# Kernel optimization log

Measured on AMD Instinct MI355X. Metric: run time of the kernel, lower is better.

Reference implementation:

```python
import jax, jax.numpy as jnp
import numpy as np

B, N, F, T = 16, 2048, 64, 32  # batch, nodes, features, frames


def setup_inputs() -> dict:
    key = jax.random.key(0)
    ks = jax.random.split(key, 6)
    return {
        "x": jax.random.normal(ks[0], (B, N, F, T), dtype=jnp.float32),
        "U_1": jax.random.normal(ks[1], (N,), dtype=jnp.float32),
        "U_2": jax.random.normal(ks[2], (F, N), dtype=jnp.float32),
        "U_3": jax.random.normal(ks[3], (F,), dtype=jnp.float32),
        "b_e": jax.random.normal(ks[4], (1, T, T), dtype=jnp.float32),
        "V_e": jax.random.normal(ks[5], (T, T), dtype=jnp.float32),
    }


def reference(x, U_1, U_2, U_3, b_e, V_e):
    # lhs = x.permute(0,3,2,1) @ U_1 @ U_2 : (B,T,F,N)@(N,)->(B,T,F); @(F,N)->(B,T,N)
    lhs = jnp.einsum("bnft,n->btf", x, U_1)
    lhs = jnp.einsum("btf,fm->btm", lhs, U_2)
    # rhs = U_3 @ x.permute(2,0,1,3) : (F,)@(F,B,N,T) -> (B,N,T)
    rhs = jnp.einsum("f,bnft->bnt", U_3, x)
    # product : (B,T,N) @ (B,N,T) -> (B,T,T)
    product = jnp.einsum("btn,bns->bts", lhs, rhs)
    # the two chained permutes in the source compose to identity
    E = jnp.einsum("ut,bts->bus", V_e, jax.nn.sigmoid(product + b_e))  # (B,T,T)
    # stable softmax-like normalization over dim=1 (the original's intent)
    E = E - jnp.max(E, axis=1, keepdims=True)
    expE = jnp.exp(E)
    return expE / jnp.sum(expE, axis=1, keepdims=True)
```

## Files before the change

kernel.cpp:

```cpp
#include <hip/hip_runtime.h>
#include <math.h>


#define BDIM 16
#define NDIM 2048
#define FDIM 64
#define TDIM 32
#define GPB  32
#define NC   16

__global__ __launch_bounds__(256) void k1_pass(
    const float* __restrict__ x, const float* __restrict__ U1,
    const float* __restrict__ U3, float* __restrict__ rhs_ws,
    float* __restrict__ lhs_part) {
  const int b    = blockIdx.x / GPB;
  const int gb   = blockIdx.x % GPB;
  const int tid  = threadIdx.x;
  const int wave = tid >> 6;
  const int lane = tid & 63;
  const int frow = lane >> 3;
  const int t4   = (lane & 7) * 4;

  float u3v[8];
#pragma unroll
  for (int i = 0; i < 8; ++i) u3v[i] = U3[frow + 8 * i];

  float4 lacc[8];
#pragma unroll
  for (int i = 0; i < 8; ++i) lacc[i] = make_float4(0.f, 0.f, 0.f, 0.f);

  const int wb = gb * 4 + wave;
  for (int n = wb; n < NDIM; n += GPB * 4) {
    const float* base = x + ((size_t)(b * NDIM + n)) * (FDIM * TDIM);
    const float u1n = U1[n];
    float4 racc = make_float4(0.f, 0.f, 0.f, 0.f);
#pragma unroll
    for (int i = 0; i < 8; ++i) {
      const float4 v = *(const float4*)(base + (frow + 8 * i) * TDIM + t4);
      lacc[i].x = fmaf(u1n, v.x, lacc[i].x);
      lacc[i].y = fmaf(u1n, v.y, lacc[i].y);
      lacc[i].z = fmaf(u1n, v.z, lacc[i].z);
      lacc[i].w = fmaf(u1n, v.w, lacc[i].w);
      racc.x = fmaf(u3v[i], v.x, racc.x);
      racc.y = fmaf(u3v[i], v.y, racc.y);
      racc.z = fmaf(u3v[i], v.z, racc.z);
      racc.w = fmaf(u3v[i], v.w, racc.w);
    }
#pragma unroll
    for (int m = 8; m <= 32; m <<= 1) {
      racc.x += __shfl_xor(racc.x, m, 64);
      racc.y += __shfl_xor(racc.y, m, 64);
      racc.z += __shfl_xor(racc.z, m, 64);
      racc.w += __shfl_xor(racc.w, m, 64);
    }
    if (frow == 0) {
      *(float4*)(rhs_ws + ((size_t)(b * NDIM + n)) * TDIM + t4) = racc;
    }
  }

  __shared__ __align__(16) float sred[4 * 2048];
  float* my = sred + wave * 2048;
#pragma unroll
  for (int i = 0; i < 8; ++i)
    *(float4*)(my + (frow + 8 * i) * TDIM + t4) = lacc[i];
  __syncthreads();
  float* outp = lhs_part + ((size_t)(b * GPB + gb)) * 2048;
  for (int p = tid; p < 2048; p += 256)
    outp[p] = sred[p] + sred[2048 + p] + sred[4096 + p] + sred[6144 + p];
}

__global__ __launch_bounds__(256) void k2_r2(
    const float* __restrict__ rhs_ws, const float* __restrict__ U2,
    const float* __restrict__ lhs_part, float* __restrict__ R2_part,
    float* __restrict__ lhs1) {
  const int b  = blockIdx.x >> 4;
  const int nc = blockIdx.x & 15;
  const int tid = threadIdx.x;

  __shared__ float srhsT[32 * 130];
  __shared__ float sU2[64 * 129];
  __shared__ __align__(16) float sAcc[4 * 2048];

  const float* rbase = rhs_ws + ((size_t)b * NDIM + nc * 128) * TDIM;
  for (int i = tid; i < 1024; i += 256) {
    const float4 v = ((const float4*)rbase)[i];
    const int n  = i >> 3;
    const int s0 = (i & 7) * 4;
    srhsT[(s0 + 0) * 130 + n] = v.x;
    srhsT[(s0 + 1) * 130 + n] = v.y;
    srhsT[(s0 + 2) * 130 + n] = v.z;
    srhsT[(s0 + 3) * 130 + n] = v.w;
  }
  const float* ubase = U2 + nc * 128;
  for (int i = tid; i < 2048; i += 256) {
    const int f = i >> 5, c = (i & 31) * 4;
    const float4 u = *(const float4*)(ubase + (size_t)f * NDIM + c);
    sU2[f * 129 + c + 0] = u.x;
    sU2[f * 129 + c + 1] = u.y;
    sU2[f * 129 + c + 2] = u.z;
    sU2[f * 129 + c + 3] = u.w;
  }

  if (tid < 128) {
    const float* lpb = lhs_part + (size_t)b * GPB * 2048 + nc * 128 + tid;
    float s = 0.f;
#pragma unroll
    for (int g = 0; g < GPB; ++g) s += lpb[g * 2048];
    lhs1[b * 2048 + nc * 128 + tid] = s;
  }
  __syncthreads();

  const int lane = tid & 63;
  const int nsub = tid >> 6;
  const int f0 = (lane >> 2) * 4;
  const int s0 = (lane & 3) * 8;
  float acc[4][8];
#pragma unroll
  for (int k = 0; k < 4; ++k)
#pragma unroll
    for (int m = 0; m < 8; ++m) acc[k][m] = 0.f;

  for (int nn = 0; nn < 32; ++nn) {
    const int n = nsub * 32 + nn;
    float u[4], v[8];
#pragma unroll
    for (int k = 0; k < 4; ++k) u[k] = sU2[(f0 + k) * 129 + n];
#pragma unroll
    for (int m = 0; m < 8; ++m) v[m] = srhsT[(s0 + m) * 130 + n];
#pragma unroll
    for (int k = 0; k < 4; ++k)
#pragma unroll
      for (int m = 0; m < 8; ++m) acc[k][m] = fmaf(u[k], v[m], acc[k][m]);
  }
#pragma unroll
  for (int k = 0; k < 4; ++k)
#pragma unroll
    for (int m = 0; m < 8; ++m)
      sAcc[nsub * 2048 + (f0 + k) * 32 + s0 + m] = acc[k][m];
  __syncthreads();

  float4* dst = (float4*)(R2_part + ((size_t)(b * NC + nc)) * 2048);
  const float4* sa = (const float4*)sAcc;
  for (int i = tid; i < 512; i += 256) {
    float4 r0 = sa[i], r1 = sa[512 + i], r2 = sa[1024 + i], r3 = sa[1536 + i];
    r0.x += r1.x + r2.x + r3.x;
    r0.y += r1.y + r2.y + r3.y;
    r0.z += r1.z + r2.z + r3.z;
    r0.w += r1.w + r2.w + r3.w;
    dst[i] = r0;
  }
}

__global__ __launch_bounds__(1024) void k3(
    const float* __restrict__ lhs1, const float* __restrict__ R2_part,
    const float* __restrict__ b_e, const float* __restrict__ V_e,
    float* __restrict__ out) {
  const int b = blockIdx.x;
  const int tid = threadIdx.x;
  __shared__ float sl[2048], sR[2048];
  __shared__ float sS[1024], sE[1024], sVe[1024], sbe[1024];
  __shared__ float smax[32], ssum[32];

  for (int p = tid; p < 2048; p += 1024) sl[p] = lhs1[b * 2048 + p];
  if (tid < 512) {
    const float* rpb = R2_part + (size_t)b * NC * 2048;
    float4 a = make_float4(0.f, 0.f, 0.f, 0.f);
#pragma unroll
    for (int nc = 0; nc < NC; ++nc) {
      const float4 v = *(const float4*)(rpb + nc * 2048 + tid * 4);
      a.x += v.x; a.y += v.y; a.z += v.z; a.w += v.w;
    }
    *(float4*)(sR + tid * 4) = a;
  }
  sVe[tid] = V_e[tid];
  sbe[tid] = b_e[tid];
  __syncthreads();

  const int t = tid >> 5, s = tid & 31;
  float p = 0.f;
#pragma unroll
  for (int f = 0; f < FDIM; ++f) p = fmaf(sl[f * 32 + t], sR[f * 32 + s], p);
  sS[t * 32 + s] = 1.f / (1.f + expf(-(p + sbe[t * 32 + s])));
  __syncthreads();
  float e = 0.f;
#pragma unroll
  for (int tt = 0; tt < 32; ++tt) e = fmaf(sVe[t * 32 + tt], sS[tt * 32 + s], e);
  sE[t * 32 + s] = e;
  __syncthreads();
  if (tid < 32) {
    float m = -1e30f;
    for (int uu = 0; uu < 32; ++uu) m = fmaxf(m, sE[uu * 32 + tid]);
    float sum = 0.f;
    for (int uu = 0; uu < 32; ++uu) sum += expf(sE[uu * 32 + tid] - m);
    smax[tid] = m;
    ssum[tid] = sum;
  }
  __syncthreads();
  out[b * 1024 + t * 32 + s] = expf(sE[t * 32 + s] - smax[s]) / ssum[s];
}

extern "C" void kernel_launch(void* const* d_in, const int* in_sizes, int n_in,
                              void* d_out, int out_size, void* d_ws, size_t ws_size,
                              hipStream_t stream) {
  const float* x   = (const float*)d_in[0];
  const float* U1  = (const float*)d_in[1];
  const float* U2  = (const float*)d_in[2];
  const float* U3  = (const float*)d_in[3];
  const float* b_e = (const float*)d_in[4];
  const float* V_e = (const float*)d_in[5];
  float* out = (float*)d_out;
  float* ws  = (float*)d_ws;

  float* rhs_ws   = ws;
  float* lhs_part = ws + 1048576;
  float* R2_part  = ws + 2097152;
  float* lhs1     = ws + 2097152 + 524288;

  k1_pass<<<BDIM * GPB, 256, 0, stream>>>(x, U1, U3, rhs_ws, lhs_part);
  k2_r2<<<BDIM * NC, 256, 0, stream>>>(rhs_ws, U2, lhs_part, R2_part, lhs1);
  k3<<<BDIM, 1024, 0, stream>>>(lhs1, R2_part, b_e, V_e, out);
}
```

Before: 386.4 us.

## Fuse final sigmoid/softmax stage into k2 via last-block atomic counter

Removes the third kernel launch by having the last block to finish each batch in k2 (detected with a per-batch atomic counter reset in k1) reduce the R2 partials and compute the sigmoid, V_e mix and column softmax. The goal is to save one launch and its gap. The tail work now runs on 256 threads instead of 1024, and the threadfence/atomic adds a little synchronisation cost.

```diff
diff --git a/kernel.cpp b/kernel.cpp
--- a/kernel.cpp
+++ b/kernel.cpp
@@ -12,7 +12,9 @@
 __global__ __launch_bounds__(256) void k1_pass(
     const float* __restrict__ x, const float* __restrict__ U1,
     const float* __restrict__ U3, float* __restrict__ rhs_ws,
-    float* __restrict__ lhs_part) {
+    float* __restrict__ lhs_part, int* __restrict__ batch_cnt) {
+  if (blockIdx.x == 0 && threadIdx.x < BDIM) batch_cnt[threadIdx.x] = 0;
+
   const int b    = blockIdx.x / GPB;
   const int gb   = blockIdx.x % GPB;
   const int tid  = threadIdx.x;
@@ -69,10 +71,12 @@
     outp[p] = sred[p] + sred[2048 + p] + sred[4096 + p] + sred[6144 + p];
 }
 
-__global__ __launch_bounds__(256) void k2_r2(
+__global__ __launch_bounds__(256) void k2_fused(
     const float* __restrict__ rhs_ws, const float* __restrict__ U2,
     const float* __restrict__ lhs_part, float* __restrict__ R2_part,
-    float* __restrict__ lhs1) {
+    float* __restrict__ lhs1, int* __restrict__ batch_cnt,
+    const float* __restrict__ b_e, const float* __restrict__ V_e,
+    float* __restrict__ out) {
   const int b  = blockIdx.x >> 4;
   const int nc = blockIdx.x & 15;
   const int tid = threadIdx.x;
@@ -80,6 +84,10 @@
   __shared__ float srhsT[32 * 130];
   __shared__ float sU2[64 * 129];
   __shared__ __align__(16) float sAcc[4 * 2048];
+  __shared__ __align__(16) float sl[2048], sR[2048];
+  __shared__ float sS[1024], sE[1024], sVe[1024], sbe[1024];
+  __shared__ float smax[32], ssum[32];
+  __shared__ int isLast;
 
   const float* rbase = rhs_ws + ((size_t)b * NDIM + nc * 128) * TDIM;
   for (int i = tid; i < 1024; i += 256) {
@@ -149,43 +157,51 @@
     r0.w += r1.w + r2.w + r3.w;
     dst[i] = r0;
   }
-}
-
-__global__ __launch_bounds__(1024) void k3(
-    const float* __restrict__ lhs1, const float* __restrict__ R2_part,
-    const float* __restrict__ b_e, const float* __restrict__ V_e,
-    float* __restrict__ out) {
-  const int b = blockIdx.x;
-  const int tid = threadIdx.x;
-  __shared__ float sl[2048], sR[2048];
-  __shared__ float sS[1024], sE[1024], sVe[1024], sbe[1024];
-  __shared__ float smax[32], ssum[32];
-
-  for (int p = tid; p < 2048; p += 1024) sl[p] = lhs1[b * 2048 + p];
-  if (tid < 512) {
-    const float* rpb = R2_part + (size_t)b * NC * 2048;
+
+  __threadfence();
+  __syncthreads();
+  if (tid == 0) {
+    const int old = atomicAdd(&batch_cnt[b], 1);
+    isLast = (old == NC - 1) ? 1 : 0;
+  }
+  __syncthreads();
+  if (!isLast) return;
+  __threadfence();
+
+  const float* rpb = R2_part + (size_t)b * NC * 2048;
+  for (int i = tid; i < 512; i += 256) {
     float4 a = make_float4(0.f, 0.f, 0.f, 0.f);
 #pragma unroll
-    for (int nc = 0; nc < NC; ++nc) {
-      const float4 v = *(const float4*)(rpb + nc * 2048 + tid * 4);
+    for (int c = 0; c < NC; ++c) {
+      const float4 v = *(const float4*)(rpb + c * 2048 + i * 4);
       a.x += v.x; a.y += v.y; a.z += v.z; a.w += v.w;
     }
-    *(float4*)(sR + tid * 4) = a;
-  }
-  sVe[tid] = V_e[tid];
-  sbe[tid] = b_e[tid];
-  __syncthreads();
-
-  const int t = tid >> 5, s = tid & 31;
-  float p = 0.f;
-#pragma unroll
-  for (int f = 0; f < FDIM; ++f) p = fmaf(sl[f * 32 + t], sR[f * 32 + s], p);
-  sS[t * 32 + s] = 1.f / (1.f + expf(-(p + sbe[t * 32 + s])));
-  __syncthreads();
-  float e = 0.f;
-#pragma unroll
-  for (int tt = 0; tt < 32; ++tt) e = fmaf(sVe[t * 32 + tt], sS[tt * 32 + s], e);
-  sE[t * 32 + s] = e;
+    *(float4*)(sR + i * 4) = a;
+  }
+  for (int p = tid; p < 2048; p += 256) sl[p] = lhs1[b * 2048 + p];
+  for (int i = tid; i < 1024; i += 256) { sVe[i] = V_e[i]; sbe[i] = b_e[i]; }
+  __syncthreads();
+
+#pragma unroll
+  for (int c = 0; c < 4; ++c) {
+    const int cell = c * 256 + tid;
+    const int t = cell >> 5, s = cell & 31;
+    float p = 0.f;
+#pragma unroll
+    for (int f = 0; f < FDIM; ++f) p = fmaf(sl[f * 32 + t], sR[f * 32 + s], p);
+    sS[cell] = 1.f / (1.f + expf(-(p + sbe[cell])));
+  }
+  __syncthreads();
+#pragma unroll
+  for (int c = 0; c < 4; ++c) {
+    const int cell = c * 256 + tid;
+    const int t = cell >> 5, s = cell & 31;
+    float e = 0.f;
+#pragma unroll
+    for (int tt = 0; tt < 32; ++tt)
+      e = fmaf(sVe[t * 32 + tt], sS[tt * 32 + s], e);
+    sE[cell] = e;
+  }
   __syncthreads();
   if (tid < 32) {
     float m = -1e30f;
@@ -196,7 +212,12 @@
     ssum[tid] = sum;
   }
   __syncthreads();
-  out[b * 1024 + t * 32 + s] = expf(sE[t * 32 + s] - smax[s]) / ssum[s];
+#pragma unroll
+  for (int c = 0; c < 4; ++c) {
+    const int cell = c * 256 + tid;
+    const int s = cell & 31;
+    out[b * 1024 + cell] = expf(sE[cell] - smax[s]) / ssum[s];
+  }
 }
 
 extern "C" void kernel_launch(void* const* d_in, const int* in_sizes, int n_in,
@@ -215,8 +236,10 @@
   float* lhs_part = ws + 1048576;
   float* R2_part  = ws + 2097152;
   float* lhs1     = ws + 2097152 + 524288;
-
-  k1_pass<<<BDIM * GPB, 256, 0, stream>>>(x, U1, U3, rhs_ws, lhs_part);
-  k2_r2<<<BDIM * NC, 256, 0, stream>>>(rhs_ws, U2, lhs_part, R2_part, lhs1);
-  k3<<<BDIM, 1024, 0, stream>>>(lhs1, R2_part, b_e, V_e, out);
+  int*   batch_cnt = (int*)(ws + 2097152 + 524288 + 32768);
+
+  k1_pass<<<BDIM * GPB, 256, 0, stream>>>(x, U1, U3, rhs_ws, lhs_part,
+                                          batch_cnt);
+  k2_fused<<<BDIM * NC, 256, 0, stream>>>(rhs_ws, U2, lhs_part, R2_part,
+                                          lhs1, batch_cnt, b_e, V_e, out);
 }
```

Result: slower. 416.0 us (+7.6%).
